# Kernel optimization log

Measured on AMD Instinct MI355X. Metric: run time of the kernel, lower is better.

Reference implementation:

```python
import jax, jax.numpy as jnp
import numpy as np

N = 100000   # nodes
E = 1250000  # edges
D = 64       # in = hidden = out channels
LN_EPS = 1e-5
L2_EPS = 1e-12


def setup_inputs() -> dict:
    key = jax.random.key(0)
    ks = jax.random.split(key, 16)
    s = 1.0 / np.sqrt(D)
    inp = {
        "x": jax.random.normal(ks[0], (N, D), jnp.float32),
        "edge_index": jax.random.randint(ks[1], (2, E), 0, N, dtype=jnp.int64),
    }
    for i in range(3):  # SAGEConv i: out = mean_aggr @ Wl + bl + x @ Wr
        inp[f"Wl{i}"] = jax.random.normal(ks[2 + 2 * i], (D, D), jnp.float32) * s
        inp[f"bl{i}"] = jnp.zeros((D,), jnp.float32)
        inp[f"Wr{i}"] = jax.random.normal(ks[3 + 2 * i], (D, D), jnp.float32) * s
    for i in range(2):  # LayerNorm after layers 0,1
        inp[f"g{i}"] = jnp.ones((D,), jnp.float32)
        inp[f"b{i}"] = jnp.zeros((D,), jnp.float32)
    return inp


def _sage_conv(x, src, dst, Wl, bl, Wr):
    # PyG SAGEConv(aggr='mean'): lin_l(mean of neighbor msgs) + lin_r(x)
    agg = jax.ops.segment_sum(x[src], dst, num_segments=N)          # [N, D]
    deg = jax.ops.segment_sum(jnp.ones((src.shape[0],), x.dtype), dst, num_segments=N)
    mean = agg / jnp.maximum(deg, 1.0)[:, None]
    return mean @ Wl + bl + x @ Wr


def _layer_norm(h, g, b):
    mu = jnp.mean(h, axis=-1, keepdims=True)
    var = jnp.mean((h - mu) ** 2, axis=-1, keepdims=True)
    return (h - mu) * jax.lax.rsqrt(var + LN_EPS) * g + b


def reference(x, edge_index, Wl0, bl0, Wr0, Wl1, bl1, Wr1, Wl2, bl2, Wr2, g0, b0, g1, b1):
    src, dst = edge_index[0], edge_index[1]
    Ws = [(Wl0, bl0, Wr0), (Wl1, bl1, Wr1), (Wl2, bl2, Wr2)]
    lns = [(g0, b0), (g1, b1)]
    h = x
    for i in range(3):
        res = h  # residual projections are Identity (equal dims)
        h = _sage_conv(h, src, dst, *Ws[i])
        if i < 2:
            h = _layer_norm(h, *lns[i])
            h = jax.nn.relu(h)
            h = h + res
            # dropout is identity in eval mode
        else:
            h = h + res
    # F.normalize(p=2, dim=1)
    nrm = jnp.sqrt(jnp.sum(h * h, axis=1, keepdims=True))
    return h / jnp.maximum(nrm, L2_EPS)
```

## Files before the change

### kernel.cpp

```cpp
#include <hip/hip_runtime.h>

#define DD   64
#define WSTR 136
#define SSTR 72
#define BSH  9
#define BNODES 512
#define BCAPSH 13

typedef unsigned int uint32;
typedef __attribute__((ext_vector_type(8))) short short8;
typedef __attribute__((ext_vector_type(4))) float f32x4;

__device__ __forceinline__ unsigned short f2bf_rne(float f) {
    uint32 u = __float_as_uint(f);
    u += 0x7fffu + ((u >> 16) & 1u);
    return (unsigned short)(u >> 16);
}
__device__ __forceinline__ float bf_lo(uint32 w) { return __uint_as_float(w << 16); }
__device__ __forceinline__ float bf_hi(uint32 w) { return __uint_as_float(w & 0xffff0000u); }
__device__ __forceinline__ float bf2f(unsigned short s) {
    return __uint_as_float(((uint32)s) << 16);
}

__global__ __launch_bounds__(256) void cvt_kernel(const float* __restrict__ x,
                                                  unsigned short* __restrict__ xb,
                                                  int n4, int* __restrict__ gCnt) {
    if (blockIdx.x == 0 && threadIdx.x < 256) gCnt[threadIdx.x] = 0;
    int i = blockIdx.x * 256 + threadIdx.x;
    if (i < n4) {
        float4 v = ((const float4*)x)[i];
        ushort4 p;
        p.x = f2bf_rne(v.x); p.y = f2bf_rne(v.y);
        p.z = f2bf_rne(v.z); p.w = f2bf_rne(v.w);
        ((ushort4*)xb)[i] = p;
    }
}

__global__ __launch_bounds__(1024) void bucket_kernel(const int* __restrict__ src,
                                                      const int* __restrict__ dst,
                                                      int* __restrict__ gCnt,
                                                      int2* __restrict__ buf, int E) {
    __shared__ int ldsCnt[256];
    __shared__ int base[256];
    const int t = threadIdx.x;
    if (t < 256) ldsCnt[t] = 0;
    __syncthreads();

    const int e0 = blockIdx.x * 4096;
    int bk[4], rk[4], sv[4], dv[4];
#pragma unroll
    for (int k = 0; k < 4; ++k) {
        int e = e0 + k * 1024 + t;
        bk[k] = -1;
        if (e < E) {
            dv[k] = dst[e];
            sv[k] = src[e];
            bk[k] = dv[k] >> BSH;
            rk[k] = atomicAdd(&ldsCnt[bk[k]], 1);
        }
    }
    __syncthreads();
    if (t < 256 && ldsCnt[t] > 0) base[t] = atomicAdd(&gCnt[t], ldsCnt[t]);
    __syncthreads();
#pragma unroll
    for (int k = 0; k < 4; ++k) {
        if (bk[k] >= 0) {
            int pos = (bk[k] << BCAPSH) + base[bk[k]] + rk[k];
            buf[pos] = make_int2(sv[k], dv[k]);
        }
    }
}

__global__ __launch_bounds__(512) void csr_build(const int2* __restrict__ buf,
                                                 const int* __restrict__ gCnt,
                                                 int* __restrict__ offsets,
                                                 int* __restrict__ csr, int N, int E) {
    __shared__ int c1[BNODES];
    __shared__ int s[BNODES];
    __shared__ int sg2[256];
    const int b = blockIdx.x;
    const int t = threadIdx.x;
    if (t < 256) sg2[t] = gCnt[t];
    c1[t] = 0;
    __syncthreads();
    for (int d = 1; d < 256; d <<= 1) {
        int v = (t < 256 && t >= d) ? sg2[t - d] : 0;
        __syncthreads();
        if (t < 256 && t >= d) sg2[t] += v;
        __syncthreads();
    }
    const int base = (b == 0) ? 0 : sg2[b - 1];
    const int cnt = gCnt[b];
    const int2* bb = buf + ((size_t)b << BCAPSH);
    for (int i = t; i < cnt; i += 512) atomicAdd(&c1[bb[i].y & (BNODES - 1)], 1);
    __syncthreads();

    int v = c1[t];
    s[t] = v;
    __syncthreads();
    for (int d = 1; d < BNODES; d <<= 1) {
        int u = (t >= d) ? s[t - d] : 0;
        __syncthreads();
        if (t >= d) s[t] += u;
        __syncthreads();
    }
    int excl = s[t] - v;
    const int node = (b << BSH) + t;
    if (node < N) offsets[node] = base + excl;
    if (b == 0 && t == 0) offsets[N] = E;
    __syncthreads();
    s[t] = excl;
    c1[t] = 0;
    __syncthreads();

    for (int i = t; i < cnt; i += 512) {
        int2 e = bb[i];
        int d = e.y & (BNODES - 1);
        int r = atomicAdd(&c1[d], 1);
        csr[base + s[d] + r] = e.x;
    }
}

template <int MODE>
__global__ __launch_bounds__(256, 4) void sage_layer(
    const unsigned short* __restrict__ hbin,
    const int* __restrict__ offsets,
    const int* __restrict__ csr,
    const float* __restrict__ Wl,
    const float* __restrict__ bl,
    const float* __restrict__ Wr,
    const float* __restrict__ g,
    const float* __restrict__ bta,
    unsigned short* __restrict__ hbout,
    float* __restrict__ out,
    int N) {
    __shared__ unsigned short sWt[64 * WSTR];
    __shared__ unsigned short sSelf[64 * SSTR];
    __shared__ unsigned short sMean[64 * SSTR];
    __shared__ float sbl[DD], sg[DD], sb[DD];

    const int t = threadIdx.x;
    const int nbase = blockIdx.x * 64;

    for (int idx = t; idx < 2 * DD * DD; idx += 256) {
        int k = idx >> 6, c = idx & 63;
        float v = (k < DD) ? Wl[idx] : Wr[idx - DD * DD];
        sWt[c * WSTR + k] = f2bf_rne(v);
    }
    if (t < DD) {
        sbl[t] = bl[t];
        if (MODE == 0) { sg[t] = g[t]; sb[t] = bta[t]; }
    }

#pragma unroll
    for (int r = 0; r < 2; ++r) {
        int idx = r * 256 + t;
        int row = idx >> 3;
        int qq  = idx & 7;
        int n   = min(nbase + row, N - 1);
        uint4 v = ((const uint4*)(hbin + (size_t)n * DD))[qq];
        *(uint4*)(&sSelf[row * SSTR + qq * 8]) = v;
    }

    {
        const int grp = t >> 3;
        const int q   = t & 7;
#pragma unroll 1
        for (int rep = 0; rep < 2; ++rep) {
            int local = grp + rep * 32;
            int node  = nbase + local;
            float a0 = 0.f, a1 = 0.f, a2 = 0.f, a3 = 0.f,
                  a4 = 0.f, a5 = 0.f, a6 = 0.f, a7 = 0.f;
            int deg = 0;
            if (node < N) {
                int off0 = offsets[node];
                int off1 = offsets[node + 1];
                deg = off1 - off0;
                for (int j = off0; j < off1; j += 8) {
                    uint4 v[8];
#pragma unroll
                    for (int s = 0; s < 8; ++s) {
                        uint4 tt = make_uint4(0u, 0u, 0u, 0u);
                        int idx = j + s;
                        if (idx < off1) {
                            int sn = __builtin_nontemporal_load(&csr[idx]);
                            tt = ((const uint4*)(hbin + (size_t)sn * DD))[q];
                        }
                        v[s] = tt;
                    }
#pragma unroll
                    for (int s = 0; s < 8; ++s) {
                        a0 += bf_lo(v[s].x); a1 += bf_hi(v[s].x);
                        a2 += bf_lo(v[s].y); a3 += bf_hi(v[s].y);
                        a4 += bf_lo(v[s].z); a5 += bf_hi(v[s].z);
                        a6 += bf_lo(v[s].w); a7 += bf_hi(v[s].w);
                    }
                }
            }
            float invd = 1.0f / fmaxf((float)deg, 1.0f);
            ushort4 pa, pb;
            pa.x = f2bf_rne(a0 * invd); pa.y = f2bf_rne(a1 * invd);
            pa.z = f2bf_rne(a2 * invd); pa.w = f2bf_rne(a3 * invd);
            pb.x = f2bf_rne(a4 * invd); pb.y = f2bf_rne(a5 * invd);
            pb.z = f2bf_rne(a6 * invd); pb.w = f2bf_rne(a7 * invd);
            *(ushort4*)(&sMean[local * SSTR + q * 8])     = pa;
            *(ushort4*)(&sMean[local * SSTR + q * 8 + 4]) = pb;
        }
    }
    __syncthreads();

    const int wave = t >> 6;
    const int lane = t & 63;
    const int quad = lane >> 4;
    const int n16  = lane & 15;
    const int lbase = wave * 16;

    short8 af[4];
    af[0] = *(const short8*)(&sMean[(lbase + n16) * SSTR + quad * 8]);
    af[1] = *(const short8*)(&sMean[(lbase + n16) * SSTR + 32 + quad * 8]);
    af[2] = *(const short8*)(&sSelf[(lbase + n16) * SSTR + quad * 8]);
    af[3] = *(const short8*)(&sSelf[(lbase + n16) * SSTR + 32 + quad * 8]);

    f32x4 acc[4];
#pragma unroll
    for (int j = 0; j < 4; ++j) {
        float bv = sbl[j * 16 + n16];
        acc[j] = (f32x4){bv, bv, bv, bv};
    }
#pragma unroll
    for (int s = 0; s < 4; ++s) {
#pragma unroll
        for (int j = 0; j < 4; ++j) {
            short8 bf = *(const short8*)(&sWt[(j * 16 + n16) * WSTR + s * 32 + quad * 8]);
            acc[j] = __builtin_amdgcn_mfma_f32_16x16x32_bf16(af[s], bf, acc[j], 0, 0, 0);
        }
    }

#pragma unroll
    for (int i = 0; i < 4; ++i) {
        const int lrow = lbase + quad * 4 + i;
        const int rr   = nbase + lrow;
        float res[4];
#pragma unroll
        for (int j = 0; j < 4; ++j)
            res[j] = bf2f(sSelf[lrow * SSTR + j * 16 + n16]);
        float o[4];
        if (MODE == 0) {
            float s4 = acc[0][i] + acc[1][i] + acc[2][i] + acc[3][i];
            s4 += __shfl_xor(s4, 1, 64);
            s4 += __shfl_xor(s4, 2, 64);
            s4 += __shfl_xor(s4, 4, 64);
            s4 += __shfl_xor(s4, 8, 64);
            float mu = s4 * (1.0f / 64.0f);
            float d0 = acc[0][i] - mu, d1 = acc[1][i] - mu,
                  d2 = acc[2][i] - mu, d3 = acc[3][i] - mu;
            float qq = d0 * d0 + d1 * d1 + d2 * d2 + d3 * d3;
            qq += __shfl_xor(qq, 1, 64);
            qq += __shfl_xor(qq, 2, 64);
            qq += __shfl_xor(qq, 4, 64);
            qq += __shfl_xor(qq, 8, 64);
            float rstd = rsqrtf(qq * (1.0f / 64.0f) + 1e-5f);
            o[0] = fmaxf(d0 * rstd * sg[ 0 + n16] + sb[ 0 + n16], 0.f) + res[0];
            o[1] = fmaxf(d1 * rstd * sg[16 + n16] + sb[16 + n16], 0.f) + res[1];
            o[2] = fmaxf(d2 * rstd * sg[32 + n16] + sb[32 + n16], 0.f) + res[2];
            o[3] = fmaxf(d3 * rstd * sg[48 + n16] + sb[48 + n16], 0.f) + res[3];
        } else {
            o[0] = acc[0][i] + res[0];
            o[1] = acc[1][i] + res[1];
            o[2] = acc[2][i] + res[2];
            o[3] = acc[3][i] + res[3];
            float qq = o[0] * o[0] + o[1] * o[1] + o[2] * o[2] + o[3] * o[3];
            qq += __shfl_xor(qq, 1, 64);
            qq += __shfl_xor(qq, 2, 64);
            qq += __shfl_xor(qq, 4, 64);
            qq += __shfl_xor(qq, 8, 64);
            float inv = 1.0f / fmaxf(sqrtf(qq), 1e-12f);
            o[0] *= inv; o[1] *= inv; o[2] *= inv; o[3] *= inv;
        }
        if (rr < N) {
#pragma unroll
            for (int j = 0; j < 4; ++j) {
                if (MODE == 0)
                    hbout[(size_t)rr * DD + j * 16 + n16] = f2bf_rne(o[j]);
                else
                    out[(size_t)rr * DD + j * 16 + n16] = o[j];
            }
        }
    }
}

extern "C" void kernel_launch(void* const* d_in, const int* in_sizes, int n_in,
                              void* d_out, int out_size, void* d_ws, size_t ws_size,
                              hipStream_t stream) {
    const float* x   = (const float*)d_in[0];
    const int*   ei  = (const int*)d_in[1];
    const float* Wl0 = (const float*)d_in[2];
    const float* bl0 = (const float*)d_in[3];
    const float* Wr0 = (const float*)d_in[4];
    const float* Wl1 = (const float*)d_in[5];
    const float* bl1 = (const float*)d_in[6];
    const float* Wr1 = (const float*)d_in[7];
    const float* Wl2 = (const float*)d_in[8];
    const float* bl2 = (const float*)d_in[9];
    const float* Wr2 = (const float*)d_in[10];
    const float* g0  = (const float*)d_in[11];
    const float* b0  = (const float*)d_in[12];
    const float* g1  = (const float*)d_in[13];
    const float* b1  = (const float*)d_in[14];

    const int N = in_sizes[0] / DD;
    const int E = in_sizes[1] / 2;
    const int* src = ei;
    const int* dst = ei + E;
    const int NB = (N + BNODES - 1) >> BSH;

    int2* bucketBuf = (int2*)d_ws;
    unsigned short* HB0 = (unsigned short*)(bucketBuf + ((size_t)256 << BCAPSH));
    unsigned short* HB1 = HB0 + (size_t)N * DD;
    int*   csr     = (int*)(HB1 + (size_t)N * DD);
    int*   offsets = csr + E;
    int*   gCnt    = offsets + (N + 1);
    float* out     = (float*)d_out;

    const int tiles = (N + 63) / 64;
    const int n4    = N * DD / 4;
    const int cgrid = (n4 + 255) / 256;
    const int bgrid = (E + 4095) / 4096;

    cvt_kernel<<<cgrid, 256, 0, stream>>>(x, HB0, n4, gCnt);
    bucket_kernel<<<bgrid, 1024, 0, stream>>>(src, dst, gCnt, bucketBuf, E);
    csr_build<<<NB, 512, 0, stream>>>(bucketBuf, gCnt, offsets, csr, N, E);

    sage_layer<0><<<tiles, 256, 0, stream>>>(HB0, offsets, csr, Wl0, bl0, Wr0,
                                             g0, b0, HB1, nullptr, N);
    sage_layer<0><<<tiles, 256, 0, stream>>>(HB1, offsets, csr, Wl1, bl1, Wr1,
                                             g1, b1, HB0, nullptr, N);
    sage_layer<1><<<tiles, 256, 0, stream>>>(HB0, offsets, csr, Wl2, bl2, Wr2,
                                             nullptr, nullptr, nullptr, out, N);
}
```

Before: 314.1 us.

## Fuse all stages into one persistent kernel with software grid barriers

Replaces the six separate launches (convert, bucket, CSR build, three SAGE layers) with a single persistent kernel sized from occupancy, separated by atomic-counter grid barriers. Each layer is split into an aggregation phase that writes the mean to a global bf16 buffer and a GEMM/LayerNorm phase that reads it back, with a barrier between them. This removes launch gaps and tail effects but adds extra global traffic for the mean buffer, more barriers, and a risk of deadlock if not all blocks are co-resident. The bucketing also switches to int4 vector loads of edges.

```diff
diff --git a/kernel.cpp b/kernel.cpp
--- a/kernel.cpp
+++ b/kernel.cpp
@@ -1,11 +1,12 @@
 #include <hip/hip_runtime.h>
 
-#define DD   64
-#define WSTR 136
-#define SSTR 72
-#define BSH  9
+#define DD     64
+#define WSTR   136
+#define BSH    9
 #define BNODES 512
 #define BCAPSH 13
+#define MAGIC  0x1357ACE5
+#define READY_OFF 256
 
 typedef unsigned int uint32;
 typedef __attribute__((ext_vector_type(8))) short short8;
@@ -22,160 +23,175 @@
     return __uint_as_float(((uint32)s) << 16);
 }
 
-__global__ __launch_bounds__(256) void cvt_kernel(const float* __restrict__ x,
-                                                  unsigned short* __restrict__ xb,
-                                                  int n4, int* __restrict__ gCnt) {
-    if (blockIdx.x == 0 && threadIdx.x < 256) gCnt[threadIdx.x] = 0;
-    int i = blockIdx.x * 256 + threadIdx.x;
-    if (i < n4) {
-        float4 v = ((const float4*)x)[i];
-        ushort4 p;
-        p.x = f2bf_rne(v.x); p.y = f2bf_rne(v.y);
-        p.z = f2bf_rne(v.z); p.w = f2bf_rne(v.w);
-        ((ushort4*)xb)[i] = p;
-    }
-}
-
-__global__ __launch_bounds__(1024) void bucket_kernel(const int* __restrict__ src,
-                                                      const int* __restrict__ dst,
-                                                      int* __restrict__ gCnt,
-                                                      int2* __restrict__ buf, int E) {
-    __shared__ int ldsCnt[256];
-    __shared__ int base[256];
-    const int t = threadIdx.x;
-    if (t < 256) ldsCnt[t] = 0;
+struct KParams {
+    const float* x;
+    const int* src;
+    const int* dst;
+    const float *Wl0, *bl0, *Wr0, *Wl1, *bl1, *Wr1, *Wl2, *bl2, *Wr2;
+    const float *g0, *b0, *g1, *b1;
+    unsigned short *HB0, *HB1, *AGGB;
+    int2* bucketBuf;
+    int *csr, *offsets, *gCnt, *bar;
+    float* out;
+    int N, E, NB, n4, ntiles;
+};
+
+struct SmemB { int cnt[256]; int base[256]; };
+struct SmemC { int c1[BNODES]; int s[BNODES]; int tmp[256]; };
+struct SmemE { unsigned short sWt[64 * WSTR]; float sbl[64]; float sg[64]; float sb[64]; };
+union SmemU { SmemB b; SmemC c; SmemE e; };
+
+__device__ __forceinline__ void gbar(int* bar, int slot, int nblk) {
     __syncthreads();
-
-    const int e0 = blockIdx.x * 4096;
-    int bk[4], rk[4], sv[4], dv[4];
-#pragma unroll
-    for (int k = 0; k < 4; ++k) {
-        int e = e0 + k * 1024 + t;
-        bk[k] = -1;
-        if (e < E) {
-            dv[k] = dst[e];
-            sv[k] = src[e];
-            bk[k] = dv[k] >> BSH;
-            rk[k] = atomicAdd(&ldsCnt[bk[k]], 1);
-        }
+    if (threadIdx.x == 0) {
+        __threadfence();
+        atomicAdd(&bar[slot * 16], 1);
+        while (atomicAdd(&bar[slot * 16], 0) < nblk) __builtin_amdgcn_s_sleep(2);
+        __threadfence();
     }
     __syncthreads();
-    if (t < 256 && ldsCnt[t] > 0) base[t] = atomicAdd(&gCnt[t], ldsCnt[t]);
+}
+
+__global__ __launch_bounds__(256, 4) void mega(KParams p) {
+    __shared__ SmemU sm;
+    const int t    = threadIdx.x;
+    const int bid  = blockIdx.x;
+    const int nblk = gridDim.x;
+
+    if (bid == 0) {
+        if (t < 16)  p.bar[t * 16] = 0;
+        if (t < 256) p.gCnt[t] = 0;
+    }
     __syncthreads();
-#pragma unroll
-    for (int k = 0; k < 4; ++k) {
-        if (bk[k] >= 0) {
-            int pos = (bk[k] << BCAPSH) + base[bk[k]] + rk[k];
-            buf[pos] = make_int2(sv[k], dv[k]);
-        }
-    }
-}
-
-__global__ __launch_bounds__(512) void csr_build(const int2* __restrict__ buf,
-                                                 const int* __restrict__ gCnt,
-                                                 int* __restrict__ offsets,
-                                                 int* __restrict__ csr, int N, int E) {
-    __shared__ int c1[BNODES];
-    __shared__ int s[BNODES];
-    __shared__ int sg2[256];
-    const int b = blockIdx.x;
-    const int t = threadIdx.x;
-    if (t < 256) sg2[t] = gCnt[t];
-    c1[t] = 0;
+    if (t == 0) {
+        if (bid == 0) { __threadfence(); atomicExch(&p.bar[READY_OFF], MAGIC); }
+        else {
+            while (atomicAdd(&p.bar[READY_OFF], 0) != MAGIC) __builtin_amdgcn_s_sleep(2);
+            __threadfence();
+        }
+    }
     __syncthreads();
-    for (int d = 1; d < 256; d <<= 1) {
-        int v = (t < 256 && t >= d) ? sg2[t - d] : 0;
-        __syncthreads();
-        if (t < 256 && t >= d) sg2[t] += v;
-        __syncthreads();
-    }
-    const int base = (b == 0) ? 0 : sg2[b - 1];
-    const int cnt = gCnt[b];
-    const int2* bb = buf + ((size_t)b << BCAPSH);
-    for (int i = t; i < cnt; i += 512) atomicAdd(&c1[bb[i].y & (BNODES - 1)], 1);
-    __syncthreads();
-
-    int v = c1[t];
-    s[t] = v;
-    __syncthreads();
-    for (int d = 1; d < BNODES; d <<= 1) {
-        int u = (t >= d) ? s[t - d] : 0;
-        __syncthreads();
-        if (t >= d) s[t] += u;
-        __syncthreads();
-    }
-    int excl = s[t] - v;
-    const int node = (b << BSH) + t;
-    if (node < N) offsets[node] = base + excl;
-    if (b == 0 && t == 0) offsets[N] = E;
-    __syncthreads();
-    s[t] = excl;
-    c1[t] = 0;
-    __syncthreads();
-
-    for (int i = t; i < cnt; i += 512) {
-        int2 e = bb[i];
-        int d = e.y & (BNODES - 1);
-        int r = atomicAdd(&c1[d], 1);
-        csr[base + s[d] + r] = e.x;
-    }
-}
-
-template <int MODE>
-__global__ __launch_bounds__(256, 4) void sage_layer(
-    const unsigned short* __restrict__ hbin,
-    const int* __restrict__ offsets,
-    const int* __restrict__ csr,
-    const float* __restrict__ Wl,
-    const float* __restrict__ bl,
-    const float* __restrict__ Wr,
-    const float* __restrict__ g,
-    const float* __restrict__ bta,
-    unsigned short* __restrict__ hbout,
-    float* __restrict__ out,
-    int N) {
-    __shared__ unsigned short sWt[64 * WSTR];
-    __shared__ unsigned short sSelf[64 * SSTR];
-    __shared__ unsigned short sMean[64 * SSTR];
-    __shared__ float sbl[DD], sg[DD], sb[DD];
-
-    const int t = threadIdx.x;
-    const int nbase = blockIdx.x * 64;
-
-    for (int idx = t; idx < 2 * DD * DD; idx += 256) {
-        int k = idx >> 6, c = idx & 63;
-        float v = (k < DD) ? Wl[idx] : Wr[idx - DD * DD];
-        sWt[c * WSTR + k] = f2bf_rne(v);
-    }
-    if (t < DD) {
-        sbl[t] = bl[t];
-        if (MODE == 0) { sg[t] = g[t]; sb[t] = bta[t]; }
-    }
-
-#pragma unroll
-    for (int r = 0; r < 2; ++r) {
-        int idx = r * 256 + t;
-        int row = idx >> 3;
-        int qq  = idx & 7;
-        int n   = min(nbase + row, N - 1);
-        uint4 v = ((const uint4*)(hbin + (size_t)n * DD))[qq];
-        *(uint4*)(&sSelf[row * SSTR + qq * 8]) = v;
-    }
+
+    for (int i = bid * 256 + t; i < p.n4; i += nblk * 256) {
+        float4 v = ((const float4*)p.x)[i];
+        ushort4 q;
+        q.x = f2bf_rne(v.x); q.y = f2bf_rne(v.y);
+        q.z = f2bf_rne(v.z); q.w = f2bf_rne(v.w);
+        ((ushort4*)p.HB0)[i] = q;
+    }
+    gbar(p.bar, 0, nblk);
 
     {
-        const int grp = t >> 3;
-        const int q   = t & 7;
-#pragma unroll 1
-        for (int rep = 0; rep < 2; ++rep) {
-            int local = grp + rep * 32;
-            int node  = nbase + local;
-            float a0 = 0.f, a1 = 0.f, a2 = 0.f, a3 = 0.f,
-                  a4 = 0.f, a5 = 0.f, a6 = 0.f, a7 = 0.f;
-            int deg = 0;
-            if (node < N) {
-                int off0 = offsets[node];
-                int off1 = offsets[node + 1];
-                deg = off1 - off0;
+        const int nchunk = (p.E + 4095) >> 12;
+        for (int c = bid; c < nchunk; c += nblk) {
+            sm.b.cnt[t] = 0;
+            __syncthreads();
+            const int e0 = c * 4096;
+            int sv[16], dv[16], rk[16];
+#pragma unroll
+            for (int k = 0; k < 4; ++k) {
+                int e = e0 + k * 1024 + t * 4;
+#pragma unroll
+                for (int u = 0; u < 4; ++u) dv[k * 4 + u] = -1;
+                if (e < p.E) {
+                    int4 s4 = *(const int4*)(p.src + e);
+                    int4 d4 = *(const int4*)(p.dst + e);
+                    sv[k * 4 + 0] = s4.x; sv[k * 4 + 1] = s4.y;
+                    sv[k * 4 + 2] = s4.z; sv[k * 4 + 3] = s4.w;
+                    dv[k * 4 + 0] = d4.x; dv[k * 4 + 1] = d4.y;
+                    dv[k * 4 + 2] = d4.z; dv[k * 4 + 3] = d4.w;
+                    rk[k * 4 + 0] = atomicAdd(&sm.b.cnt[d4.x >> BSH], 1);
+                    rk[k * 4 + 1] = atomicAdd(&sm.b.cnt[d4.y >> BSH], 1);
+                    rk[k * 4 + 2] = atomicAdd(&sm.b.cnt[d4.z >> BSH], 1);
+                    rk[k * 4 + 3] = atomicAdd(&sm.b.cnt[d4.w >> BSH], 1);
+                }
+            }
+            __syncthreads();
+            if (sm.b.cnt[t] > 0) sm.b.base[t] = atomicAdd(&p.gCnt[t], sm.b.cnt[t]);
+            __syncthreads();
+#pragma unroll
+            for (int k = 0; k < 16; ++k) {
+                if (dv[k] >= 0) {
+                    int bk = dv[k] >> BSH;
+                    int pos = (bk << BCAPSH) + sm.b.base[bk] + rk[k];
+                    p.bucketBuf[pos] = make_int2(sv[k], dv[k]);
+                }
+            }
+            __syncthreads();
+        }
+    }
+    gbar(p.bar, 1, nblk);
+
+    {
+        for (int b = bid; b < p.NB; b += nblk) {
+            sm.c.tmp[t] = (t < p.NB) ? p.gCnt[t] : 0;
+            __syncthreads();
+            for (int d = 1; d < 256; d <<= 1) {
+                int v = (t >= d) ? sm.c.tmp[t - d] : 0;
+                __syncthreads();
+                if (t >= d) sm.c.tmp[t] += v;
+                __syncthreads();
+            }
+            const int base = (b == 0) ? 0 : sm.c.tmp[b - 1];
+            __syncthreads();
+
+            sm.c.c1[t] = 0; sm.c.c1[t + 256] = 0;
+            __syncthreads();
+            const int cnt = p.gCnt[b];
+            const int2* bb = p.bucketBuf + ((size_t)b << BCAPSH);
+            for (int i = t; i < cnt; i += 256)
+                atomicAdd(&sm.c.c1[bb[i].y & (BNODES - 1)], 1);
+            __syncthreads();
+
+            int a0 = sm.c.c1[2 * t], a1 = sm.c.c1[2 * t + 1];
+            int pp = a0 + a1;
+            sm.c.tmp[t] = pp;
+            __syncthreads();
+            for (int d = 1; d < 256; d <<= 1) {
+                int v = (t >= d) ? sm.c.tmp[t - d] : 0;
+                __syncthreads();
+                if (t >= d) sm.c.tmp[t] += v;
+                __syncthreads();
+            }
+            int ex = sm.c.tmp[t] - pp;
+            sm.c.s[2 * t]     = ex;
+            sm.c.s[2 * t + 1] = ex + a0;
+            int n0g = (b << BSH) + 2 * t;
+            if (n0g < p.N)     p.offsets[n0g]     = base + ex;
+            if (n0g + 1 < p.N) p.offsets[n0g + 1] = base + ex + a0;
+            if (b == 0 && t == 0) p.offsets[p.N] = p.E;
+            __syncthreads();
+            sm.c.c1[t] = 0; sm.c.c1[t + 256] = 0;
+            __syncthreads();
+            for (int i = t; i < cnt; i += 256) {
+                int2 e = bb[i];
+                int d = e.y & (BNODES - 1);
+                int r = atomicAdd(&sm.c.c1[d], 1);
+                p.csr[base + sm.c.s[d] + r] = e.x;
+            }
+            __syncthreads();
+        }
+    }
+    gbar(p.bar, 2, nblk);
+
+    const unsigned short* HBin = p.HB0;
+    unsigned short* HBout = p.HB1;
+    int barSlot = 3;
+
+    for (int layer = 0; layer < 3; ++layer) {
+        const float *Wl, *bl, *Wr, *gg, *bb2;
+        if (layer == 0)      { Wl = p.Wl0; bl = p.bl0; Wr = p.Wr0; gg = p.g0; bb2 = p.b0; }
+        else if (layer == 1) { Wl = p.Wl1; bl = p.bl1; Wr = p.Wr1; gg = p.g1; bb2 = p.b1; }
+        else                 { Wl = p.Wl2; bl = p.bl2; Wr = p.Wr2; gg = nullptr; bb2 = nullptr; }
+
+        {
+            const int q = t & 7;
+            const int gstep = nblk * 32;
+            for (int node = bid * 32 + (t >> 3); node < p.N; node += gstep) {
+                const int off0 = p.offsets[node];
+                const int off1 = p.offsets[node + 1];
+                float a0 = 0.f, a1 = 0.f, a2 = 0.f, a3 = 0.f,
+                      a4 = 0.f, a5 = 0.f, a6 = 0.f, a7 = 0.f;
                 for (int j = off0; j < off1; j += 8) {
                     uint4 v[8];
 #pragma unroll
@@ -183,8 +199,8 @@
                         uint4 tt = make_uint4(0u, 0u, 0u, 0u);
                         int idx = j + s;
                         if (idx < off1) {
-                            int sn = __builtin_nontemporal_load(&csr[idx]);
-                            tt = ((const uint4*)(hbin + (size_t)sn * DD))[q];
+                            int sn = __builtin_nontemporal_load(&p.csr[idx]);
+                            tt = ((const uint4*)(HBin + (size_t)sn * DD))[q];
                         }
                         v[s] = tt;
                     }
@@ -196,145 +212,165 @@
                         a6 += bf_lo(v[s].w); a7 += bf_hi(v[s].w);
                     }
                 }
-            }
-            float invd = 1.0f / fmaxf((float)deg, 1.0f);
-            ushort4 pa, pb;
-            pa.x = f2bf_rne(a0 * invd); pa.y = f2bf_rne(a1 * invd);
-            pa.z = f2bf_rne(a2 * invd); pa.w = f2bf_rne(a3 * invd);
-            pb.x = f2bf_rne(a4 * invd); pb.y = f2bf_rne(a5 * invd);
-            pb.z = f2bf_rne(a6 * invd); pb.w = f2bf_rne(a7 * invd);
-            *(ushort4*)(&sMean[local * SSTR + q * 8])     = pa;
-            *(ushort4*)(&sMean[local * SSTR + q * 8 + 4]) = pb;
-        }
-    }
-    __syncthreads();
-
-    const int wave = t >> 6;
-    const int lane = t & 63;
-    const int quad = lane >> 4;
-    const int n16  = lane & 15;
-    const int lbase = wave * 16;
-
-    short8 af[4];
-    af[0] = *(const short8*)(&sMean[(lbase + n16) * SSTR + quad * 8]);
-    af[1] = *(const short8*)(&sMean[(lbase + n16) * SSTR + 32 + quad * 8]);
-    af[2] = *(const short8*)(&sSelf[(lbase + n16) * SSTR + quad * 8]);
-    af[3] = *(const short8*)(&sSelf[(lbase + n16) * SSTR + 32 + quad * 8]);
-
-    f32x4 acc[4];
-#pragma unroll
-    for (int j = 0; j < 4; ++j) {
-        float bv = sbl[j * 16 + n16];
-        acc[j] = (f32x4){bv, bv, bv, bv};
-    }
-#pragma unroll
-    for (int s = 0; s < 4; ++s) {
-#pragma unroll
-        for (int j = 0; j < 4; ++j) {
-            short8 bf = *(const short8*)(&sWt[(j * 16 + n16) * WSTR + s * 32 + quad * 8]);
-            acc[j] = __builtin_amdgcn_mfma_f32_16x16x32_bf16(af[s], bf, acc[j], 0, 0, 0);
-        }
-    }
-
-#pragma unroll
-    for (int i = 0; i < 4; ++i) {
-        const int lrow = lbase + quad * 4 + i;
-        const int rr   = nbase + lrow;
-        float res[4];
-#pragma unroll
-        for (int j = 0; j < 4; ++j)
-            res[j] = bf2f(sSelf[lrow * SSTR + j * 16 + n16]);
-        float o[4];
-        if (MODE == 0) {
-            float s4 = acc[0][i] + acc[1][i] + acc[2][i] + acc[3][i];
-            s4 += __shfl_xor(s4, 1, 64);
-            s4 += __shfl_xor(s4, 2, 64);
-            s4 += __shfl_xor(s4, 4, 64);
-            s4 += __shfl_xor(s4, 8, 64);
-            float mu = s4 * (1.0f / 64.0f);
-            float d0 = acc[0][i] - mu, d1 = acc[1][i] - mu,
-                  d2 = acc[2][i] - mu, d3 = acc[3][i] - mu;
-            float qq = d0 * d0 + d1 * d1 + d2 * d2 + d3 * d3;
-            qq += __shfl_xor(qq, 1, 64);
-            qq += __shfl_xor(qq, 2, 64);
-            qq += __shfl_xor(qq, 4, 64);
-            qq += __shfl_xor(qq, 8, 64);
-            float rstd = rsqrtf(qq * (1.0f / 64.0f) + 1e-5f);
-            o[0] = fmaxf(d0 * rstd * sg[ 0 + n16] + sb[ 0 + n16], 0.f) + res[0];
-            o[1] = fmaxf(d1 * rstd * sg[16 + n16] + sb[16 + n16], 0.f) + res[1];
-            o[2] = fmaxf(d2 * rstd * sg[32 + n16] + sb[32 + n16], 0.f) + res[2];
-            o[3] = fmaxf(d3 * rstd * sg[48 + n16] + sb[48 + n16], 0.f) + res[3];
-        } else {
-            o[0] = acc[0][i] + res[0];
-            o[1] = acc[1][i] + res[1];
-            o[2] = acc[2][i] + res[2];
-            o[3] = acc[3][i] + res[3];
-            float qq = o[0] * o[0] + o[1] * o[1] + o[2] * o[2] + o[3] * o[3];
-            qq += __shfl_xor(qq, 1, 64);
-            qq += __shfl_xor(qq, 2, 64);
-            qq += __shfl_xor(qq, 4, 64);
-            qq += __shfl_xor(qq, 8, 64);
-            float inv = 1.0f / fmaxf(sqrtf(qq), 1e-12f);
-            o[0] *= inv; o[1] *= inv; o[2] *= inv; o[3] *= inv;
-        }
-        if (rr < N) {
-#pragma unroll
-            for (int j = 0; j < 4; ++j) {
-                if (MODE == 0)
-                    hbout[(size_t)rr * DD + j * 16 + n16] = f2bf_rne(o[j]);
-                else
-                    out[(size_t)rr * DD + j * 16 + n16] = o[j];
-            }
-        }
+                float invd = 1.0f / fmaxf((float)(off1 - off0), 1.0f);
+                unsigned short* orow = p.AGGB + (size_t)node * DD + q * 8;
+                ushort4 pa, pb;
+                pa.x = f2bf_rne(a0 * invd); pa.y = f2bf_rne(a1 * invd);
+                pa.z = f2bf_rne(a2 * invd); pa.w = f2bf_rne(a3 * invd);
+                pb.x = f2bf_rne(a4 * invd); pb.y = f2bf_rne(a5 * invd);
+                pb.z = f2bf_rne(a6 * invd); pb.w = f2bf_rne(a7 * invd);
+                *(ushort4*)(orow)     = pa;
+                *(ushort4*)(orow + 4) = pb;
+            }
+        }
+        gbar(p.bar, barSlot++, nblk);
+
+        {
+            for (int idx = t; idx < 2 * DD * DD; idx += 256) {
+                int k = idx >> 6, c = idx & 63;
+                float v = (k < DD) ? Wl[idx] : Wr[idx - DD * DD];
+                sm.e.sWt[c * WSTR + k] = f2bf_rne(v);
+            }
+            if (t < DD) {
+                sm.e.sbl[t] = bl[t];
+                if (layer < 2) { sm.e.sg[t] = gg[t]; sm.e.sb[t] = bb2[t]; }
+            }
+            __syncthreads();
+
+            const int wave = t >> 6;
+            const int lane = t & 63;
+            const int quad = lane >> 4;
+            const int n16  = lane & 15;
+
+            for (int tile = bid; tile < p.ntiles; tile += nblk) {
+                const int nbase = tile * 64 + wave * 16;
+                const int arow  = min(nbase + n16, p.N - 1);
+                const unsigned short* mrow = p.AGGB + (size_t)arow * DD;
+                const unsigned short* hrow = HBin   + (size_t)arow * DD;
+                short8 af0 = *(const short8*)(mrow + quad * 8);
+                short8 af1 = *(const short8*)(mrow + 32 + quad * 8);
+                short8 af2 = *(const short8*)(hrow + quad * 8);
+                short8 af3 = *(const short8*)(hrow + 32 + quad * 8);
+
+                f32x4 acc[4];
+#pragma unroll
+                for (int j = 0; j < 4; ++j) {
+                    float bv = sm.e.sbl[j * 16 + n16];
+                    acc[j] = (f32x4){bv, bv, bv, bv};
+                }
+#pragma unroll
+                for (int j = 0; j < 4; ++j) {
+                    short8 bf;
+                    bf = *(const short8*)(&sm.e.sWt[(j * 16 + n16) * WSTR + 0 * 32 + quad * 8]);
+                    acc[j] = __builtin_amdgcn_mfma_f32_16x16x32_bf16(af0, bf, acc[j], 0, 0, 0);
+                    bf = *(const short8*)(&sm.e.sWt[(j * 16 + n16) * WSTR + 1 * 32 + quad * 8]);
+                    acc[j] = __builtin_amdgcn_mfma_f32_16x16x32_bf16(af1, bf, acc[j], 0, 0, 0);
+                    bf = *(const short8*)(&sm.e.sWt[(j * 16 + n16) * WSTR + 2 * 32 + quad * 8]);
+                    acc[j] = __builtin_amdgcn_mfma_f32_16x16x32_bf16(af2, bf, acc[j], 0, 0, 0);
+                    bf = *(const short8*)(&sm.e.sWt[(j * 16 + n16) * WSTR + 3 * 32 + quad * 8]);
+                    acc[j] = __builtin_amdgcn_mfma_f32_16x16x32_bf16(af3, bf, acc[j], 0, 0, 0);
+                }
+
+#pragma unroll
+                for (int i = 0; i < 4; ++i) {
+                    const int rr = nbase + quad * 4 + i;
+                    const int rc = min(rr, p.N - 1);
+                    float res[4];
+#pragma unroll
+                    for (int j = 0; j < 4; ++j)
+                        res[j] = bf2f(HBin[(size_t)rc * DD + j * 16 + n16]);
+                    float o[4];
+                    if (layer < 2) {
+                        float s4 = acc[0][i] + acc[1][i] + acc[2][i] + acc[3][i];
+                        s4 += __shfl_xor(s4, 1, 64);
+                        s4 += __shfl_xor(s4, 2, 64);
+                        s4 += __shfl_xor(s4, 4, 64);
+                        s4 += __shfl_xor(s4, 8, 64);
+                        float mu = s4 * (1.0f / 64.0f);
+                        float d0 = acc[0][i] - mu, d1 = acc[1][i] - mu,
+                              d2 = acc[2][i] - mu, d3 = acc[3][i] - mu;
+                        float qq = d0 * d0 + d1 * d1 + d2 * d2 + d3 * d3;
+                        qq += __shfl_xor(qq, 1, 64);
+                        qq += __shfl_xor(qq, 2, 64);
+                        qq += __shfl_xor(qq, 4, 64);
+                        qq += __shfl_xor(qq, 8, 64);
+                        float rstd = rsqrtf(qq * (1.0f / 64.0f) + 1e-5f);
+                        o[0] = fmaxf(d0 * rstd * sm.e.sg[ 0 + n16] + sm.e.sb[ 0 + n16], 0.f) + res[0];
+                        o[1] = fmaxf(d1 * rstd * sm.e.sg[16 + n16] + sm.e.sb[16 + n16], 0.f) + res[1];
+                        o[2] = fmaxf(d2 * rstd * sm.e.sg[32 + n16] + sm.e.sb[32 + n16], 0.f) + res[2];
+                        o[3] = fmaxf(d3 * rstd * sm.e.sg[48 + n16] + sm.e.sb[48 + n16], 0.f) + res[3];
+                        if (rr < p.N) {
+#pragma unroll
+                            for (int j = 0; j < 4; ++j)
+                                HBout[(size_t)rr * DD + j * 16 + n16] = f2bf_rne(o[j]);
+                        }
+                    } else {
+                        o[0] = acc[0][i] + res[0];
+                        o[1] = acc[1][i] + res[1];
+                        o[2] = acc[2][i] + res[2];
+                        o[3] = acc[3][i] + res[3];
+                        float qq = o[0] * o[0] + o[1] * o[1] + o[2] * o[2] + o[3] * o[3];
+                        qq += __shfl_xor(qq, 1, 64);
+                        qq += __shfl_xor(qq, 2, 64);
+                        qq += __shfl_xor(qq, 4, 64);
+                        qq += __shfl_xor(qq, 8, 64);
+                        float inv = 1.0f / fmaxf(sqrtf(qq), 1e-12f);
+                        if (rr < p.N) {
+#pragma unroll
+                            for (int j = 0; j < 4; ++j)
+                                p.out[(size_t)rr * DD + j * 16 + n16] = o[j] * inv;
+                        }
+                    }
+                }
+            }
+        }
+        if (layer < 2) gbar(p.bar, barSlot++, nblk);
+
+        const unsigned short* tp = HBin;
+        HBin  = HBout;
+        HBout = (unsigned short*)tp;
     }
 }
 
 extern "C" void kernel_launch(void* const* d_in, const int* in_sizes, int n_in,
                               void* d_out, int out_size, void* d_ws, size_t ws_size,
                               hipStream_t stream) {
-    const float* x   = (const float*)d_in[0];
-    const int*   ei  = (const int*)d_in[1];
-    const float* Wl0 = (const float*)d_in[2];
-    const float* bl0 = (const float*)d_in[3];
-    const float* Wr0 = (const float*)d_in[4];
-    const float* Wl1 = (const float*)d_in[5];
-    const float* bl1 = (const float*)d_in[6];
-    const float* Wr1 = (const float*)d_in[7];
-    const float* Wl2 = (const float*)d_in[8];
-    const float* bl2 = (const float*)d_in[9];
-    const float* Wr2 = (const float*)d_in[10];
-    const float* g0  = (const float*)d_in[11];
-    const float* b0  = (const float*)d_in[12];
-    const float* g1  = (const float*)d_in[13];
-    const float* b1  = (const float*)d_in[14];
+    KParams kp;
+    kp.x   = (const float*)d_in[0];
+    const int* ei = (const int*)d_in[1];
+    kp.Wl0 = (const float*)d_in[2];  kp.bl0 = (const float*)d_in[3];
+    kp.Wr0 = (const float*)d_in[4];
+    kp.Wl1 = (const float*)d_in[5];  kp.bl1 = (const float*)d_in[6];
+    kp.Wr1 = (const float*)d_in[7];
+    kp.Wl2 = (const float*)d_in[8];  kp.bl2 = (const float*)d_in[9];
+    kp.Wr2 = (const float*)d_in[10];
+    kp.g0  = (const float*)d_in[11]; kp.b0  = (const float*)d_in[12];
+    kp.g1  = (const float*)d_in[13]; kp.b1  = (const float*)d_in[14];
 
     const int N = in_sizes[0] / DD;
     const int E = in_sizes[1] / 2;
-    const int* src = ei;
-    const int* dst = ei + E;
-    const int NB = (N + BNODES - 1) >> BSH;
-
-    int2* bucketBuf = (int2*)d_ws;
-    unsigned short* HB0 = (unsigned short*)(bucketBuf + ((size_t)256 << BCAPSH));
-    unsigned short* HB1 = HB0 + (size_t)N * DD;
-    int*   csr     = (int*)(HB1 + (size_t)N * DD);
-    int*   offsets = csr + E;
-    int*   gCnt    = offsets + (N + 1);
-    float* out     = (float*)d_out;
-
-    const int tiles = (N + 63) / 64;
-    const int n4    = N * DD / 4;
-    const int cgrid = (n4 + 255) / 256;
-    const int bgrid = (E + 4095) / 4096;
-
-    cvt_kernel<<<cgrid, 256, 0, stream>>>(x, HB0, n4, gCnt);
-    bucket_kernel<<<bgrid, 1024, 0, stream>>>(src, dst, gCnt, bucketBuf, E);
-    csr_build<<<NB, 512, 0, stream>>>(bucketBuf, gCnt, offsets, csr, N, E);
-
-    sage_layer<0><<<tiles, 256, 0, stream>>>(HB0, offsets, csr, Wl0, bl0, Wr0,
-                                             g0, b0, HB1, nullptr, N);
-    sage_layer<0><<<tiles, 256, 0, stream>>>(HB1, offsets, csr, Wl1, bl1, Wr1,
-                                             g1, b1, HB0, nullptr, N);
-    sage_layer<1><<<tiles, 256, 0, stream>>>(HB0, offsets, csr, Wl2, bl2, Wr2,
-                                             nullptr, nullptr, nullptr, out, N);
-}
+    kp.N = N; kp.E = E;
+    kp.src = ei;
+    kp.dst = ei + E;
+    kp.NB = (N + BNODES - 1) >> BSH;
+    kp.n4 = N * DD / 4;
+    kp.ntiles = (N + 63) / 64;
+    kp.out = (float*)d_out;
+
+    kp.bucketBuf = (int2*)d_ws;
+    kp.HB0  = (unsigned short*)(kp.bucketBuf + ((size_t)256 << BCAPSH));
+    kp.HB1  = kp.HB0 + (size_t)N * DD;
+    kp.AGGB = kp.HB1 + (size_t)N * DD;
+    kp.csr  = (int*)(kp.AGGB + (size_t)N * DD);
+    kp.offsets = kp.csr + E;
+    kp.gCnt = kp.offsets + (N + 1);
+    kp.bar  = kp.gCnt + 256;
+
+    int occ = 0;
+    hipError_t err = hipOccupancyMaxActiveBlocksPerMultiprocessor(&occ, (const void*)mega, 256, 0);
+    if (err != hipSuccess || occ < 1) occ = 4;
+    if (occ > 8) occ = 8;
+    const int nblk = occ * 256;
+
+    mega<<<nblk, 256, 0, stream>>>(kp);
+}
```

New measurement: 859.4 us. 2.74x slower.
